# Optimization experiments

Hardware: AMD Instinct MI355X
Metric: run time of the kernel (lower is better)

## Reference

```python
import jax, jax.numpy as jnp
import numpy as np

B, D, K, H, E, Z = 64, 25000, 16, 128, 256, 32


def setup_inputs() -> dict:
    key = jax.random.key(0)
    ks = jax.random.split(key, 10)
    s = 0.02
    return {
        "x": jax.random.normal(ks[0], (B, D), jnp.float32),
        "mask": jax.random.randint(ks[1], (B, D), 0, 2, jnp.int32),
        "feat_emb": jax.random.normal(ks[2], (D, K), jnp.float32),          # feature_embedding [D,K]
        "feat_bias": jnp.zeros((D, 1), jnp.float32),                        # feature_bias [D,1]
        "W1": jax.random.normal(ks[3], (1 + K + 1, H), jnp.float32) * s,    # h_layer linear 1 (in,out)
        "b1": jnp.zeros((H,), jnp.float32),
        "W2": jax.random.normal(ks[4], (H, K), jnp.float32) * s,            # h_layer linear 2
        "b2": jnp.zeros((K,), jnp.float32),
        "We1": jax.random.normal(ks[5], (K, E), jnp.float32) * s,           # encoder_mlp linear 1
        "be1": jnp.zeros((E,), jnp.float32),
        "We2": jax.random.normal(ks[6], (E, 2 * Z), jnp.float32) * s,       # encoder_mlp linear 2
        "be2": jnp.zeros((2 * Z,), jnp.float32),
    }


def reference(x, mask, feat_emb, feat_bias, W1, b1, W2, b2, We1, be1, We2, be2):
    b, d = x.shape
    k = feat_emb.shape[1]
    # Build per-(sample, feature) input rows: [x_bd, F_d(K), bias_d] -> [B, D, 1+K+1]
    h_in = jnp.concatenate(
        [
            x[:, :, None],
            jnp.broadcast_to(feat_emb[None, :, :], (b, d, k)),
            jnp.broadcast_to(feat_bias[None, :, :], (b, d, 1)),
        ],
        axis=-1,
    )
    # Shared small MLP (h_layer), dropout is identity at rate 0.0
    h = jax.nn.relu(h_in @ W1 + b1)          # [B, D, H]
    h = jax.nn.relu(h @ W2 + b2)             # [B, D, K]
    # Masked sum pooling over features
    c = jnp.sum(h * mask.astype(h.dtype)[:, :, None], axis=1)  # [B, K]
    # encoder_mlp
    enc = jax.nn.relu(c @ We1 + be1) @ We2 + be2                # [B, 2Z]
    mu, logvar = jnp.split(enc, 2, axis=-1)
    return mu, logvar
```

## Files before the change

kernel.cpp:

```cpp
#include <hip/hip_runtime.h>
#include <hip/hip_bf16.h>

#define B 64
#define D 25000
#define K 16
#define H 128
#define E 256
#define Z 32
#define DTILE 10
#define NBLK (D / DTILE)
#define NREP 8
#define NTILE ((D + 63) / 64)

#define REP_BYTES (NREP * B * K * 4)
#define HI_OFF    REP_BYTES
#define W1F_OFF   (HI_OFF + H * K * 2)
#define MT_OFF    (W1F_OFF + 8 * 64 * 8 * 2)

typedef __attribute__((ext_vector_type(8))) _Float16 half8;
typedef __attribute__((ext_vector_type(4))) _Float16 hv4;
typedef __attribute__((ext_vector_type(2))) _Float16 hv2;
typedef __attribute__((ext_vector_type(4))) float f32x4;

__global__ __launch_bounds__(256) void prep_kernel(
    const int* __restrict__ mask, const float* __restrict__ W1,
    const float* __restrict__ b1, const float* __restrict__ W2,
    float* __restrict__ rep, _Float16* __restrict__ hiW2,
    _Float16* __restrict__ w1f, _Float16* __restrict__ mTh)
{
    const int t = threadIdx.x;
    const int bid = blockIdx.x;
    if (bid < NREP) {
        for (int i = t; i < B * K; i += 256) rep[bid * B * K + i] = 0.f;
    } else if (bid == NREP) {
        for (int i = t; i < H * K; i += 256) {
            int j = i & 7, n = (i >> 3) & 15, g = (i >> 7) & 3, s = i >> 9;
            int k = s * 32 + g * 8 + j;
            hiW2[i] = (_Float16)W2[k * K + n];
        }
    } else if (bid == NREP + 1) {
        for (int i = t; i < 8 * 64 * 8; i += 256) {
            int j = i & 7, lane = (i >> 3) & 63, c = i >> 9;
            int g = lane >> 4, n = lane & 15;
            int k = g * 8 + j, h = c * 16 + n;
            float v;
            if (k < 16)       v = W1[(1 + k) * H + h];
            else if (k == 16) v = W1[17 * H + h];
            else if (k == 17) v = b1[h];
            else              v = 0.f;
            w1f[i] = (_Float16)v;
        }
    } else {
        __shared__ float tm[64 * 65];
        const int dt0 = (bid - NREP - 2) * 64;
        const int dn  = min(64, D - dt0);
        for (int i = t; i < 64 * 64; i += 256) {
            int bb = i >> 6, dd = i & 63;
            if (dd < dn) tm[dd * 65 + bb] = (float)mask[(size_t)bb * D + dt0 + dd];
        }
        __syncthreads();
        for (int i = t; i < dn * 64; i += 256) {
            int dd = i >> 6, bb = i & 63;
            mTh[(size_t)(dt0 + dd) * 64 + bb] = (_Float16)tm[dd * 65 + bb];
        }
    }
}

__global__ __launch_bounds__(256) void partial_main_kernel(
    const float* __restrict__ x, const float* __restrict__ feat_emb,
    const float* __restrict__ feat_bias, const float* __restrict__ W1,
    const float* __restrict__ b2, const _Float16* __restrict__ hiW2,
    const _Float16* __restrict__ w1f, const _Float16* __restrict__ mTh,
    float* __restrict__ rep)
{
    __shared__ __align__(16) _Float16 sG4[4][DTILE * H];

    const int t    = threadIdx.x;
    const int d0   = blockIdx.x * DTILE;
    const int lane = t & 63;
    const int wv   = t >> 6;
    const int g    = lane >> 4;
    const int n    = lane & 15;
    _Float16* sGw  = sG4[wv];

    {
        const int dA = d0 + n;
        const int dAc = min(dA, D - 1);
        union AF { half8 v; _Float16 e[8]; } af;
        if (g < 2) {
            const float4* fe = (const float4*)&feat_emb[(size_t)dAc * K + g * 8];
            float4 u0 = fe[0], u1 = fe[1];
            af.e[0] = (_Float16)u0.x; af.e[1] = (_Float16)u0.y;
            af.e[2] = (_Float16)u0.z; af.e[3] = (_Float16)u0.w;
            af.e[4] = (_Float16)u1.x; af.e[5] = (_Float16)u1.y;
            af.e[6] = (_Float16)u1.z; af.e[7] = (_Float16)u1.w;
        } else if (g == 2) {
            af.e[0] = (_Float16)feat_bias[dAc];
            af.e[1] = (_Float16)1.f;
            #pragma unroll
            for (int j = 2; j < 8; ++j) af.e[j] = (_Float16)0.f;
        } else {
            #pragma unroll
            for (int j = 0; j < 8; ++j) af.e[j] = (_Float16)0.f;
        }
        #pragma unroll
        for (int c = 0; c < 8; ++c) {
            half8 bf = *(const half8*)(w1f + (((c << 6) + lane) << 3));
            f32x4 C = {0.f, 0.f, 0.f, 0.f};
            C = __builtin_amdgcn_mfma_f32_16x16x32_f16(af.v, bf, C, 0, 0, 0);
            #pragma unroll
            for (int r = 0; r < 4; ++r) {
                const int m2 = g * 4 + r;
                if (m2 < DTILE) sGw[m2 * H + c * 16 + n] = (_Float16)C[r];
            }
        }
    }

    const int sample = wv * 16 + n;
    const int moff   = wv * 16 + g * 4;

    const float* xrow = x + (size_t)sample * D + d0;
    hv2 xh[DTILE / 2];
    #pragma unroll
    for (int i = 0; i < DTILE / 2; ++i) {
        float2 xv = *(const float2*)(xrow + 2 * i);
        xh[i] = (hv2){(_Float16)xv.x, (_Float16)xv.y};
    }
    hv4 mv[DTILE];
    #pragma unroll
    for (int dd = 0; dd < DTILE; ++dd)
        mv[dd] = *(const hv4*)(mTh + (size_t)(d0 + dd) * B + moff);

    half8 Bf[4];
    #pragma unroll
    for (int s = 0; s < 4; ++s)
        Bf[s] = *(const half8*)(hiW2 + (((s * 4 + g) * 16 + n) << 3));
    hv2 w0h[4][4];
    #pragma unroll
    for (int s = 0; s < 4; ++s) {
        const float4* wp = (const float4*)&W1[s * 32 + g * 8];
        float4 a0 = wp[0], a1 = wp[1];
        w0h[s][0] = (hv2){(_Float16)a0.x, (_Float16)a0.y};
        w0h[s][1] = (hv2){(_Float16)a0.z, (_Float16)a0.w};
        w0h[s][2] = (hv2){(_Float16)a1.x, (_Float16)a1.y};
        w0h[s][3] = (hv2){(_Float16)a1.z, (_Float16)a1.w};
    }
    const float b2n = b2[n];
    const hv2 zeroh = {(_Float16)0.f, (_Float16)0.f};

    f32x4 cacc = {0.f, 0.f, 0.f, 0.f};
    const _Float16* gb0 = sGw + g * 8;

    #pragma unroll
    for (int i = 0; i < DTILE / 2; ++i) {
        const int dd0 = 2 * i, dd1 = 2 * i + 1;
        const hv2 xa = {xh[i].x, xh[i].x};
        const hv2 xb = {xh[i].y, xh[i].y};
        f32x4 c1a = {b2n, b2n, b2n, b2n};
        f32x4 c1b = {b2n, b2n, b2n, b2n};
        #pragma unroll
        for (int s = 0; s < 4; ++s) {
            union GA { half8 v; hv2 p[4]; };
            GA ga, gb, A0, A1;
            ga.v = *(const half8*)(gb0 + dd0 * H + s * 32);
            gb.v = *(const half8*)(gb0 + dd1 * H + s * 32);
            #pragma unroll
            for (int p = 0; p < 4; ++p) {
                hv2 h0 = __builtin_elementwise_fma(xa, w0h[s][p], ga.p[p]);
                hv2 h1 = __builtin_elementwise_fma(xb, w0h[s][p], gb.p[p]);
                A0.p[p] = __builtin_elementwise_max(h0, zeroh);
                A1.p[p] = __builtin_elementwise_max(h1, zeroh);
            }
            c1a = __builtin_amdgcn_mfma_f32_16x16x32_f16(A0.v, Bf[s], c1a, 0, 0, 0);
            c1b = __builtin_amdgcn_mfma_f32_16x16x32_f16(A1.v, Bf[s], c1b, 0, 0, 0);
        }
        cacc[0] = fmaf((float)mv[dd0].x, fmaxf(c1a[0], 0.f), fmaf((float)mv[dd1].x, fmaxf(c1b[0], 0.f), cacc[0]));
        cacc[1] = fmaf((float)mv[dd0].y, fmaxf(c1a[1], 0.f), fmaf((float)mv[dd1].y, fmaxf(c1b[1], 0.f), cacc[1]));
        cacc[2] = fmaf((float)mv[dd0].z, fmaxf(c1a[2], 0.f), fmaf((float)mv[dd1].z, fmaxf(c1b[2], 0.f), cacc[2]));
        cacc[3] = fmaf((float)mv[dd0].w, fmaxf(c1a[3], 0.f), fmaf((float)mv[dd1].w, fmaxf(c1b[3], 0.f), cacc[3]));
    }

    float* crep = rep + (size_t)(blockIdx.x & (NREP - 1)) * (B * K);
    #pragma unroll
    for (int r = 0; r < 4; ++r)
        atomicAdd(&crep[(moff + r) * K + n], cacc[r]);
}

__global__ __launch_bounds__(256) void partial_enc_kernel(
    const float* __restrict__ rep, const float* __restrict__ We1,
    const float* __restrict__ be1, const float* __restrict__ We2,
    const float* __restrict__ be2, float* __restrict__ out)
{
    const int b = blockIdx.x;
    const int t = threadIdx.x;
    __shared__ float sc[K];
    __shared__ float st1[E];
    __shared__ float red[256];

    {
        const int k = t & 15, grp = t >> 4;
        red[t] = (grp < NREP) ? rep[grp * (B * K) + b * K + k] : 0.f;
    }
    __syncthreads();
    if (t < K) {
        float s2 = 0.f;
        #pragma unroll
        for (int q = 0; q < 16; ++q) s2 += red[q * 16 + t];
        sc[t] = s2;
    }
    __syncthreads();

    {
        float acc = be1[t];
        #pragma unroll
        for (int k = 0; k < K; ++k)
            acc = fmaf(sc[k], We1[k * E + t], acc);
        st1[t] = fmaxf(acc, 0.f);
    }
    __syncthreads();

    const int j = t & 63, seg = t >> 6;
    float acc = 0.f;
    #pragma unroll 4
    for (int e = seg * 64; e < seg * 64 + 64; ++e)
        acc = fmaf(st1[e], We2[e * 64 + j], acc);
    red[t] = acc;
    __syncthreads();

    if (t < 64) {
        float v = red[j] + red[64 + j] + red[128 + j] + red[192 + j] + be2[j];
        if (j < Z) out[b * Z + j] = v;
        else       out[B * Z + b * Z + (j - Z)] = v;
    }
}

extern "C" void kernel_launch(void* const* d_in, const int* in_sizes, int n_in,
                              void* d_out, int out_size, void* d_ws, size_t ws_size,
                              hipStream_t stream) {
    const float* x         = (const float*)d_in[0];
    const int*   mask      = (const int*)  d_in[1];
    const float* feat_emb  = (const float*)d_in[2];
    const float* feat_bias = (const float*)d_in[3];
    const float* W1        = (const float*)d_in[4];
    const float* b1        = (const float*)d_in[5];
    const float* W2        = (const float*)d_in[6];
    const float* b2        = (const float*)d_in[7];
    const float* We1       = (const float*)d_in[8];
    const float* be1       = (const float*)d_in[9];
    const float* We2       = (const float*)d_in[10];
    const float* be2       = (const float*)d_in[11];

    float*     rep  = (float*)d_ws;
    _Float16*  hiW2 = (_Float16*)((char*)d_ws + HI_OFF);
    _Float16*  w1f  = (_Float16*)((char*)d_ws + W1F_OFF);
    _Float16*  mTh  = (_Float16*)((char*)d_ws + MT_OFF);

    prep_kernel<<<NREP + 2 + NTILE, 256, 0, stream>>>(
        mask, W1, b1, W2, rep, hiW2, w1f, mTh);
    partial_main_kernel<<<NBLK, 256, 0, stream>>>(
        x, feat_emb, feat_bias, W1, b2, hiW2, w1f, mTh, rep);
    partial_enc_kernel<<<B, 256, 0, stream>>>(
        rep, We1, be1, We2, be2, (float*)d_out);
}
```

Baseline: 122.6 us.

## Enlarge feature tile and share first-layer table and mask across block in LDS

Each block now covers 40 features instead of 10. The first-layer feature contribution is computed once per block by three waves into a single shared LDS table, where before each of the four waves built its own copy. The mask tile is staged into LDS with coalesced loads, and x is read as float4. This removes redundant per-wave MFMA prologue work and cuts the number of blocks and atomics, but it adds a block-wide barrier and leaves fewer blocks to spread across CUs.

```diff
diff --git a/kernel.cpp b/kernel.cpp
--- a/kernel.cpp
+++ b/kernel.cpp
@@ -7,7 +7,7 @@
 #define H 128
 #define E 256
 #define Z 32
-#define DTILE 10
+#define DTILE 40
 #define NBLK (D / DTILE)
 #define NREP 8
 #define NTILE ((D + 63) / 64)
@@ -73,7 +73,8 @@
     const _Float16* __restrict__ w1f, const _Float16* __restrict__ mTh,
     float* __restrict__ rep)
 {
-    __shared__ __align__(16) _Float16 sG4[4][DTILE * H];
+    __shared__ __align__(16) _Float16 sGh[DTILE * H];
+    __shared__ __align__(16) _Float16 sMh[DTILE * B];
 
     const int t    = threadIdx.x;
     const int d0   = blockIdx.x * DTILE;
@@ -81,10 +82,17 @@
     const int wv   = t >> 6;
     const int g    = lane >> 4;
     const int n    = lane & 15;
-    _Float16* sGw  = sG4[wv];
 
     {
-        const int dA = d0 + n;
+        const unsigned* ms = (const unsigned*)(mTh + (size_t)d0 * B);
+        unsigned* md = (unsigned*)sMh;
+        #pragma unroll
+        for (int i = t; i < DTILE * B / 2; i += 256) md[i] = ms[i];
+    }
+
+    if (wv < 3) {
+        const int rg = wv;
+        const int dA = d0 + rg * 16 + n;
         const int dAc = min(dA, D - 1);
         union AF { half8 v; _Float16 e[8]; } af;
         if (g < 2) {
@@ -110,26 +118,21 @@
             C = __builtin_amdgcn_mfma_f32_16x16x32_f16(af.v, bf, C, 0, 0, 0);
             #pragma unroll
             for (int r = 0; r < 4; ++r) {
-                const int m2 = g * 4 + r;
-                if (m2 < DTILE) sGw[m2 * H + c * 16 + n] = (_Float16)C[r];
+                const int dd = rg * 16 + g * 4 + r;
+                if (dd < DTILE) sGh[dd * H + c * 16 + n] = (_Float16)C[r];
             }
         }
     }
 
     const int sample = wv * 16 + n;
-    const int moff   = wv * 16 + g * 4;
-
     const float* xrow = x + (size_t)sample * D + d0;
     hv2 xh[DTILE / 2];
     #pragma unroll
-    for (int i = 0; i < DTILE / 2; ++i) {
-        float2 xv = *(const float2*)(xrow + 2 * i);
-        xh[i] = (hv2){(_Float16)xv.x, (_Float16)xv.y};
-    }
-    hv4 mv[DTILE];
-    #pragma unroll
-    for (int dd = 0; dd < DTILE; ++dd)
-        mv[dd] = *(const hv4*)(mTh + (size_t)(d0 + dd) * B + moff);
+    for (int i = 0; i < DTILE / 4; ++i) {
+        float4 xv = *(const float4*)(xrow + 4 * i);
+        xh[2 * i]     = (hv2){(_Float16)xv.x, (_Float16)xv.y};
+        xh[2 * i + 1] = (hv2){(_Float16)xv.z, (_Float16)xv.w};
+    }
 
     half8 Bf[4];
     #pragma unroll
@@ -147,9 +150,11 @@
     }
     const float b2n = b2[n];
     const hv2 zeroh = {(_Float16)0.f, (_Float16)0.f};
+    __syncthreads();
 
     f32x4 cacc = {0.f, 0.f, 0.f, 0.f};
-    const _Float16* gb0 = sGw + g * 8;
+    const int moff = wv * 16 + g * 4;
+    const _Float16* gb0 = sGh + g * 8;
 
     #pragma unroll
     for (int i = 0; i < DTILE / 2; ++i) {
@@ -174,10 +179,12 @@
             c1a = __builtin_amdgcn_mfma_f32_16x16x32_f16(A0.v, Bf[s], c1a, 0, 0, 0);
             c1b = __builtin_amdgcn_mfma_f32_16x16x32_f16(A1.v, Bf[s], c1b, 0, 0, 0);
         }
-        cacc[0] = fmaf((float)mv[dd0].x, fmaxf(c1a[0], 0.f), fmaf((float)mv[dd1].x, fmaxf(c1b[0], 0.f), cacc[0]));
-        cacc[1] = fmaf((float)mv[dd0].y, fmaxf(c1a[1], 0.f), fmaf((float)mv[dd1].y, fmaxf(c1b[1], 0.f), cacc[1]));
-        cacc[2] = fmaf((float)mv[dd0].z, fmaxf(c1a[2], 0.f), fmaf((float)mv[dd1].z, fmaxf(c1b[2], 0.f), cacc[2]));
-        cacc[3] = fmaf((float)mv[dd0].w, fmaxf(c1a[3], 0.f), fmaf((float)mv[dd1].w, fmaxf(c1b[3], 0.f), cacc[3]));
+        hv4 m0 = *(const hv4*)&sMh[dd0 * B + moff];
+        hv4 m1 = *(const hv4*)&sMh[dd1 * B + moff];
+        cacc[0] = fmaf((float)m0.x, fmaxf(c1a[0], 0.f), fmaf((float)m1.x, fmaxf(c1b[0], 0.f), cacc[0]));
+        cacc[1] = fmaf((float)m0.y, fmaxf(c1a[1], 0.f), fmaf((float)m1.y, fmaxf(c1b[1], 0.f), cacc[1]));
+        cacc[2] = fmaf((float)m0.z, fmaxf(c1a[2], 0.f), fmaf((float)m1.z, fmaxf(c1b[2], 0.f), cacc[2]));
+        cacc[3] = fmaf((float)m0.w, fmaxf(c1a[3], 0.f), fmaf((float)m1.w, fmaxf(c1b[3], 0.f), cacc[3]));
     }
 
     float* crep = rep + (size_t)(blockIdx.x & (NREP - 1)) * (B * K);
```

Result: faster. 116.5 us (-5.0%).
